# Kernel optimization log

Measured on AMD Instinct MI355X. Metric: run time of the kernel, lower is better.

Reference implementation:

```python
import jax, jax.numpy as jnp
import numpy as np

N2 = 524288   # raw batch (2B)
F = 256       # raw feature dim; concat of halves -> D = 2F
D = 512       # input_dim (gated feature dim)
H_GATE = 64
H_EXP = 128


def _init(key, shape, fan_in):
    return jax.random.normal(key, shape, jnp.float32) / np.sqrt(fan_in)


def setup_inputs() -> dict:
    key = jax.random.key(0)
    ks = jax.random.split(key, 13)
    x = jax.random.normal(ks[0], (N2, F), jnp.float32)
    # gate: Linear(D,64) -> ReLU -> Linear(64,2)
    gw1 = _init(ks[1], (D, H_GATE), D)
    gb1 = jnp.zeros((H_GATE,), jnp.float32)
    gw2 = _init(ks[2], (H_GATE, 2), H_GATE)
    gb2 = jnp.zeros((2,), jnp.float32)
    # expert_a: Linear(D,128) -> ReLU -> Linear(128,2)
    aw1 = _init(ks[3], (D, H_EXP), D)
    ab1 = jnp.zeros((H_EXP,), jnp.float32)
    aw2 = _init(ks[4], (H_EXP, 2), H_EXP)
    ab2 = jnp.zeros((2,), jnp.float32)
    # expert_b: same shapes
    bw1 = _init(ks[5], (D, H_EXP), D)
    bb1 = jnp.zeros((H_EXP,), jnp.float32)
    bw2 = _init(ks[6], (H_EXP, 2), H_EXP)
    bb2 = jnp.zeros((2,), jnp.float32)
    return dict(x=x, gw1=gw1, gb1=gb1, gw2=gw2, gb2=gb2,
                aw1=aw1, ab1=ab1, aw2=aw2, ab2=ab2,
                bw1=bw1, bb1=bb1, bw2=bw2, bb2=bb2)


def reference(x, gw1, gb1, gw2, gb2, aw1, ab1, aw2, ab2, bw1, bb1, bw2, bb2):
    # backbone = identity; concat first and second batch halves along features
    n = x.shape[0]
    xf = jnp.concatenate([x[: n // 2], x[n // 2 :]], axis=1)  # [B, D]
    # hard gate: argmax over 2 logits
    gate_logits = jax.nn.relu(xf @ gw1 + gb1) @ gw2 + gb2  # [B, 2]
    gate_idx = jnp.argmax(gate_logits, axis=1)  # [B]
    # run both tiny experts densely, then mask (same math as masked dispatch)
    out_a = jax.nn.relu(xf @ aw1 + ab1) @ aw2 + ab2  # [B, 2]
    out_b = jax.nn.relu(xf @ bw1 + bb1) @ bw2 + bb2  # [B, 2]
    m_a = (gate_idx == 0)[:, None]
    # rows routed to expert_a fill cols 0:2, rows routed to expert_b fill cols 2:4
    return jnp.concatenate(
        [jnp.where(m_a, out_a, 0.0), jnp.where(m_a, 0.0, out_b)], axis=1
    )  # [B, 4]
```

## Files before the change

kernel.cpp:

```cpp
#include <hip/hip_runtime.h>
#include <hip/hip_bf16.h>

#define HALF_ROWS 262144
#define TAU 0.04f
#define BT_OFF 1024
#define LIST_OFF (BT_OFF + 320 * 512 * 2)

typedef __attribute__((ext_vector_type(8))) short s16x8;
typedef __attribute__((ext_vector_type(4))) unsigned short u16x4;
typedef __attribute__((ext_vector_type(4))) float f32x4;

__device__ __forceinline__ unsigned short f2bf(float f) {
  union { float f; unsigned u; } v; v.f = f;
  unsigned r = v.u + 0x7fffu + ((v.u >> 16) & 1u);
  return (unsigned short)(r >> 16);
}

__global__ void moe_prep(const float* __restrict__ gw1, const float* __restrict__ aw1,
                         const float* __restrict__ bw1, unsigned short* __restrict__ Bf,
                         unsigned* __restrict__ cnt) {
  if (blockIdx.x == 0 && threadIdx.x == 0) *cnt = 0u;
  int idx = blockIdx.x * 512 + threadIdx.x;
  int j = idx & 7, l = (idx >> 3) & 63, ks = (idx >> 9) & 15, cb = idx >> 13;
  int col = cb * 16 + (l & 15);
  int k = ks * 32 + ((l >> 4) << 3) + j;
  float v;
  if (col < 64)       v = gw1[k * 64 + col];
  else if (col < 192) v = aw1[k * 128 + (col - 64)];
  else                v = bw1[k * 128 + (col - 192)];
  Bf[idx] = f2bf(v);
}

__global__ __launch_bounds__(512, 4) void moe_main(
    const float* __restrict__ x, const unsigned short* __restrict__ Bf,
    const float* __restrict__ gb1, const float* __restrict__ gw2, const float* __restrict__ gb2,
    const float* __restrict__ ab1, const float* __restrict__ aw2, const float* __restrict__ ab2,
    const float* __restrict__ bb1, const float* __restrict__ bw2, const float* __restrict__ bb2,
    float* __restrict__ out, unsigned* __restrict__ cnt, unsigned* __restrict__ list, int cap) {
  __shared__ unsigned short A[64 * 512];

  const int tid = threadIdx.x;
  const long br = (long)blockIdx.x * 64;

#pragma unroll 1
  for (int rnd = 0; rnd < 2; ++rnd) {
    f32x4 v[8];
#pragma unroll
    for (int u = 0; u < 8; ++u) {
      int i = tid + (rnd * 8 + u) * 512;
      int row = i >> 7, kq = i & 127;
      long roff = br + row + ((kq >> 6) ? (long)HALF_ROWS : 0L);
      v[u] = *(const f32x4*)(x + roff * 256 + (kq & 63) * 4);
    }
#pragma unroll
    for (int u = 0; u < 8; ++u) {
      int i = tid + (rnd * 8 + u) * 512;
      int row = i >> 7, kq = i & 127;
      u16x4 p;
      p[0] = f2bf(v[u][0]); p[1] = f2bf(v[u][1]);
      p[2] = f2bf(v[u][2]); p[3] = f2bf(v[u][3]);
      int byte = (row * 1024 + kq * 8) ^ ((row & 7) << 4);
      *(u16x4*)((char*)A + byte) = p;
    }
  }
  __syncthreads();

  const int w = tid >> 6, l = tid & 63;
  const int wr = w >> 2, wc = w & 3;
  const int lo = l & 15, hi = l >> 4;

  f32x4 acc[2][5];
#pragma unroll
  for (int i = 0; i < 2; i++)
#pragma unroll
    for (int j = 0; j < 5; j++) acc[i][j] = (f32x4){0.f, 0.f, 0.f, 0.f};

#pragma unroll 2
  for (int ks = 0; ks < 16; ++ks) {
    s16x8 bfr[5], afr[2];
#pragma unroll
    for (int ct = 0; ct < 5; ++ct)
      bfr[ct] = *(const s16x8*)(Bf + (((size_t)((wc * 5 + ct) * 16 + ks)) << 9) + l * 8);
#pragma unroll
    for (int rt = 0; rt < 2; ++rt) {
      int row = wr * 32 + rt * 16 + lo;
      int byte = (row * 1024 + ks * 64 + hi * 16) ^ ((l & 7) << 4);
      afr[rt] = *(const s16x8*)((const char*)A + byte);
    }
#pragma unroll
    for (int rt = 0; rt < 2; ++rt)
#pragma unroll
      for (int ct = 0; ct < 5; ++ct)
        acc[rt][ct] = __builtin_amdgcn_mfma_f32_16x16x32_bf16(
            afr[rt], bfr[ct], acc[rt][ct], 0, 0, 0);
  }
  __syncthreads();

  float* part = (float*)A;
  float b1v[5], w0v[5], w1v[5];
  int head[5];
#pragma unroll
  for (int ct = 0; ct < 5; ++ct) {
    int c0 = wc * 80 + ct * 16;
    int col = c0 + lo;
    int hd = c0 < 64 ? 0 : (c0 < 192 ? 1 : 2);
    head[ct] = hd;
    if (hd == 0)      { b1v[ct] = gb1[col];           w0v[ct] = gw2[col * 2];       w1v[ct] = gw2[col * 2 + 1]; }
    else if (hd == 1) { int c = col - 64;  b1v[ct] = ab1[c]; w0v[ct] = aw2[c * 2]; w1v[ct] = aw2[c * 2 + 1]; }
    else              { int c = col - 192; b1v[ct] = bb1[c]; w0v[ct] = bw2[c * 2]; w1v[ct] = bw2[c * 2 + 1]; }
  }
#pragma unroll
  for (int rt = 0; rt < 2; ++rt) {
    float pg0[4] = {0,0,0,0}, pg1[4] = {0,0,0,0};
    float pa0[4] = {0,0,0,0}, pa1[4] = {0,0,0,0};
    float pq0[4] = {0,0,0,0}, pq1[4] = {0,0,0,0};
#pragma unroll
    for (int ct = 0; ct < 5; ++ct)
#pragma unroll
      for (int j = 0; j < 4; ++j) {
        float h = fmaxf(acc[rt][ct][j] + b1v[ct], 0.f);
        float t0 = h * w0v[ct], t1 = h * w1v[ct];
        if (head[ct] == 0)      { pg0[j] += t0; pg1[j] += t1; }
        else if (head[ct] == 1) { pa0[j] += t0; pa1[j] += t1; }
        else                    { pq0[j] += t0; pq1[j] += t1; }
      }
#pragma unroll
    for (int m = 1; m < 16; m <<= 1)
#pragma unroll
      for (int j = 0; j < 4; ++j) {
        pg0[j] += __shfl_xor(pg0[j], m); pg1[j] += __shfl_xor(pg1[j], m);
        pa0[j] += __shfl_xor(pa0[j], m); pa1[j] += __shfl_xor(pa1[j], m);
        pq0[j] += __shfl_xor(pq0[j], m); pq1[j] += __shfl_xor(pq1[j], m);
      }
    if (lo == 0) {
#pragma unroll
      for (int j = 0; j < 4; ++j) {
        int r = wr * 32 + rt * 16 + hi * 4 + j;
        float* pp = part + (r * 4 + wc) * 6;
        pp[0] = pg0[j]; pp[1] = pg1[j]; pp[2] = pa0[j];
        pp[3] = pa1[j]; pp[4] = pq0[j]; pp[5] = pq1[j];
      }
    }
  }
  __syncthreads();

  if (tid < 64) {
    float g0 = 0, g1 = 0, a0 = 0, a1 = 0, e0 = 0, e1 = 0;
#pragma unroll
    for (int k2 = 0; k2 < 4; k2++) {
      float* pp = part + (tid * 4 + k2) * 6;
      g0 += pp[0]; g1 += pp[1]; a0 += pp[2]; a1 += pp[3]; e0 += pp[4]; e1 += pp[5];
    }
    float gl0 = g0 + gb2[0], gl1 = g1 + gb2[1];
    float fa0 = a0 + ab2[0], fa1 = a1 + ab2[1];
    float fb0 = e0 + bb2[0], fb1 = e1 + bb2[1];
    bool m0 = gl0 >= gl1;
    long grow = br + tid;
    f32x4 o;
    o[0] = m0 ? fa0 : 0.f; o[1] = m0 ? fa1 : 0.f;
    o[2] = m0 ? 0.f : fb0; o[3] = m0 ? 0.f : fb1;
    *(f32x4*)(out + grow * 4) = o;
    float diff = gl0 - gl1;
    if (fabsf(diff) < TAU && cap > 0) {
      unsigned u = atomicAdd(cnt, 1u);
      if (u < (unsigned)cap) {
        unsigned* e = list + (size_t)u * 8;
        e[0] = (unsigned)grow;
        float* ef = (float*)(e + 4);
        ef[0] = fa0; ef[1] = fa1; ef[2] = fb0; ef[3] = fb1;
      }
    }
  }
}

__global__ void moe_fixup(const float* __restrict__ x,
                          const float* __restrict__ gw1, const float* __restrict__ gb1,
                          const float* __restrict__ gw2, const float* __restrict__ gb2,
                          float* __restrict__ out, const unsigned* __restrict__ cnt,
                          const unsigned* __restrict__ list, int cap) {
  unsigned n = *cnt;
  if (n > (unsigned)cap) n = (unsigned)cap;
  const int l = threadIdx.x & 63;
  const int wid = blockIdx.x * (blockDim.x >> 6) + (threadIdx.x >> 6);
  const int nw = gridDim.x * (blockDim.x >> 6);
  for (unsigned e = wid; e < n; e += nw) {
    const unsigned* ent = list + (size_t)e * 8;
    unsigned row = ent[0];
    const float* ef = (const float*)(ent + 4);
    const float* xr0 = x + (long)row * 256;
    const float* xr1 = x + ((long)row + HALF_ROWS) * 256;
    double a0 = 0.0, a1 = 0.0, a2 = 0.0, a3 = 0.0;
#pragma unroll 4
    for (int d = 0; d < 256; d += 4) {
      a0 += (double)xr0[d]     * (double)gw1[d * 64 + l];
      a1 += (double)xr0[d + 1] * (double)gw1[(d + 1) * 64 + l];
      a2 += (double)xr0[d + 2] * (double)gw1[(d + 2) * 64 + l];
      a3 += (double)xr0[d + 3] * (double)gw1[(d + 3) * 64 + l];
    }
#pragma unroll 4
    for (int d = 0; d < 256; d += 4) {
      a0 += (double)xr1[d]     * (double)gw1[(d + 256) * 64 + l];
      a1 += (double)xr1[d + 1] * (double)gw1[(d + 257) * 64 + l];
      a2 += (double)xr1[d + 2] * (double)gw1[(d + 258) * 64 + l];
      a3 += (double)xr1[d + 3] * (double)gw1[(d + 259) * 64 + l];
    }
    double h = a0 + a1 + a2 + a3 + (double)gb1[l];
    h = h > 0.0 ? h : 0.0;
    double t0 = h * (double)gw2[l * 2];
    double t1 = h * (double)gw2[l * 2 + 1];
#pragma unroll
    for (int m = 1; m < 64; m <<= 1) {
      t0 += __shfl_xor(t0, m);
      t1 += __shfl_xor(t1, m);
    }
    if (l == 0) {
      bool m0 = (t0 + (double)gb2[0]) >= (t1 + (double)gb2[1]);
      f32x4 o;
      o[0] = m0 ? ef[0] : 0.f; o[1] = m0 ? ef[1] : 0.f;
      o[2] = m0 ? 0.f : ef[2]; o[3] = m0 ? 0.f : ef[3];
      *(f32x4*)(out + (size_t)row * 4) = o;
    }
  }
}

extern "C" void kernel_launch(void* const* d_in, const int* in_sizes, int n_in,
                              void* d_out, int out_size, void* d_ws, size_t ws_size,
                              hipStream_t stream) {
  const float* x   = (const float*)d_in[0];
  const float* gw1 = (const float*)d_in[1];
  const float* gb1 = (const float*)d_in[2];
  const float* gw2 = (const float*)d_in[3];
  const float* gb2 = (const float*)d_in[4];
  const float* aw1 = (const float*)d_in[5];
  const float* ab1 = (const float*)d_in[6];
  const float* aw2 = (const float*)d_in[7];
  const float* ab2 = (const float*)d_in[8];
  const float* bw1 = (const float*)d_in[9];
  const float* bb1 = (const float*)d_in[10];
  const float* bw2 = (const float*)d_in[11];
  const float* bb2 = (const float*)d_in[12];
  float* out = (float*)d_out;

  unsigned char* ws = (unsigned char*)d_ws;
  unsigned* cnt = (unsigned*)ws;
  unsigned short* Bf = (unsigned short*)(ws + BT_OFF);
  unsigned* list = (unsigned*)(ws + LIST_OFF);
  long cap_l = ((long)ws_size - (long)LIST_OFF) / 32;
  int cap = cap_l < 0 ? 0 : (cap_l > 262144 ? 262144 : (int)cap_l);

  moe_prep<<<320, 512, 0, stream>>>(gw1, aw1, bw1, Bf, cnt);
  moe_main<<<4096, 512, 0, stream>>>(x, Bf, gb1, gw2, gb2, ab1, aw2, ab2,
                                     bb1, bw2, bb2, out, cnt, list, cap);
  moe_fixup<<<1024, 256, 0, stream>>>(x, gw1, gb1, gw2, gb2, out, cnt, list, cap);
}
```

Before: 311.6 us.

## Make moe_main persistent over eight panels with register-prefetch of next panel

Each block now handles eight consecutive 64-row panels instead of one, and the grid shrinks to 512 blocks. The next panel's x tile is loaded into registers while the current panel's MFMA and epilogue run, then converted and written to LDS afterwards. The aim is to hide global load latency behind compute and to amortize per-block setup such as the bias and weight loads. In exchange it holds 16 extra f32x4 registers per thread, lowers launch bounds to 2 blocks per CU, and uses fewer blocks, which may leave CUs under-filled.

```diff
diff --git a/kernel.cpp b/kernel.cpp
--- a/kernel.cpp
+++ b/kernel.cpp
@@ -31,72 +31,21 @@
   Bf[idx] = f2bf(v);
 }
 
-__global__ __launch_bounds__(512, 4) void moe_main(
+__global__ __launch_bounds__(512, 2) void moe_main(
     const float* __restrict__ x, const unsigned short* __restrict__ Bf,
     const float* __restrict__ gb1, const float* __restrict__ gw2, const float* __restrict__ gb2,
     const float* __restrict__ ab1, const float* __restrict__ aw2, const float* __restrict__ ab2,
     const float* __restrict__ bb1, const float* __restrict__ bw2, const float* __restrict__ bb2,
     float* __restrict__ out, unsigned* __restrict__ cnt, unsigned* __restrict__ list, int cap) {
   __shared__ unsigned short A[64 * 512];
+  __shared__ float part[64 * 4 * 6];
 
   const int tid = threadIdx.x;
-  const long br = (long)blockIdx.x * 64;
-
-#pragma unroll 1
-  for (int rnd = 0; rnd < 2; ++rnd) {
-    f32x4 v[8];
-#pragma unroll
-    for (int u = 0; u < 8; ++u) {
-      int i = tid + (rnd * 8 + u) * 512;
-      int row = i >> 7, kq = i & 127;
-      long roff = br + row + ((kq >> 6) ? (long)HALF_ROWS : 0L);
-      v[u] = *(const f32x4*)(x + roff * 256 + (kq & 63) * 4);
-    }
-#pragma unroll
-    for (int u = 0; u < 8; ++u) {
-      int i = tid + (rnd * 8 + u) * 512;
-      int row = i >> 7, kq = i & 127;
-      u16x4 p;
-      p[0] = f2bf(v[u][0]); p[1] = f2bf(v[u][1]);
-      p[2] = f2bf(v[u][2]); p[3] = f2bf(v[u][3]);
-      int byte = (row * 1024 + kq * 8) ^ ((row & 7) << 4);
-      *(u16x4*)((char*)A + byte) = p;
-    }
-  }
-  __syncthreads();
-
   const int w = tid >> 6, l = tid & 63;
   const int wr = w >> 2, wc = w & 3;
   const int lo = l & 15, hi = l >> 4;
-
-  f32x4 acc[2][5];
-#pragma unroll
-  for (int i = 0; i < 2; i++)
-#pragma unroll
-    for (int j = 0; j < 5; j++) acc[i][j] = (f32x4){0.f, 0.f, 0.f, 0.f};
-
-#pragma unroll 2
-  for (int ks = 0; ks < 16; ++ks) {
-    s16x8 bfr[5], afr[2];
-#pragma unroll
-    for (int ct = 0; ct < 5; ++ct)
-      bfr[ct] = *(const s16x8*)(Bf + (((size_t)((wc * 5 + ct) * 16 + ks)) << 9) + l * 8);
-#pragma unroll
-    for (int rt = 0; rt < 2; ++rt) {
-      int row = wr * 32 + rt * 16 + lo;
-      int byte = (row * 1024 + ks * 64 + hi * 16) ^ ((l & 7) << 4);
-      afr[rt] = *(const s16x8*)((const char*)A + byte);
-    }
-#pragma unroll
-    for (int rt = 0; rt < 2; ++rt)
-#pragma unroll
-      for (int ct = 0; ct < 5; ++ct)
-        acc[rt][ct] = __builtin_amdgcn_mfma_f32_16x16x32_bf16(
-            afr[rt], bfr[ct], acc[rt][ct], 0, 0, 0);
-  }
-  __syncthreads();
-
-  float* part = (float*)A;
+  const int p0 = blockIdx.x * 8;
+
   float b1v[5], w0v[5], w1v[5];
   int head[5];
 #pragma unroll
@@ -109,67 +58,132 @@
     else if (hd == 1) { int c = col - 64;  b1v[ct] = ab1[c]; w0v[ct] = aw2[c * 2]; w1v[ct] = aw2[c * 2 + 1]; }
     else              { int c = col - 192; b1v[ct] = bb1[c]; w0v[ct] = bw2[c * 2]; w1v[ct] = bw2[c * 2 + 1]; }
   }
-#pragma unroll
-  for (int rt = 0; rt < 2; ++rt) {
-    float pg0[4] = {0,0,0,0}, pg1[4] = {0,0,0,0};
-    float pa0[4] = {0,0,0,0}, pa1[4] = {0,0,0,0};
-    float pq0[4] = {0,0,0,0}, pq1[4] = {0,0,0,0};
-#pragma unroll
-    for (int ct = 0; ct < 5; ++ct)
-#pragma unroll
-      for (int j = 0; j < 4; ++j) {
-        float h = fmaxf(acc[rt][ct][j] + b1v[ct], 0.f);
-        float t0 = h * w0v[ct], t1 = h * w1v[ct];
-        if (head[ct] == 0)      { pg0[j] += t0; pg1[j] += t1; }
-        else if (head[ct] == 1) { pa0[j] += t0; pa1[j] += t1; }
-        else                    { pq0[j] += t0; pq1[j] += t1; }
-      }
-#pragma unroll
-    for (int m = 1; m < 16; m <<= 1)
-#pragma unroll
-      for (int j = 0; j < 4; ++j) {
-        pg0[j] += __shfl_xor(pg0[j], m); pg1[j] += __shfl_xor(pg1[j], m);
-        pa0[j] += __shfl_xor(pa0[j], m); pa1[j] += __shfl_xor(pa1[j], m);
-        pq0[j] += __shfl_xor(pq0[j], m); pq1[j] += __shfl_xor(pq1[j], m);
-      }
-    if (lo == 0) {
-#pragma unroll
-      for (int j = 0; j < 4; ++j) {
-        int r = wr * 32 + rt * 16 + hi * 4 + j;
-        float* pp = part + (r * 4 + wc) * 6;
-        pp[0] = pg0[j]; pp[1] = pg1[j]; pp[2] = pa0[j];
-        pp[3] = pa1[j]; pp[4] = pq0[j]; pp[5] = pq1[j];
-      }
-    }
-  }
+
+  f32x4 st[16];
+  auto issueP = [&](int panel) {
+    long br = (long)panel * 64;
+#pragma unroll
+    for (int u = 0; u < 16; ++u) {
+      int i = tid + u * 512;
+      int row = i >> 7, kq = i & 127;
+      long roff = br + row + ((kq >> 6) ? (long)HALF_ROWS : 0L);
+      st[u] = *(const f32x4*)(x + roff * 256 + (kq & 63) * 4);
+    }
+  };
+  auto commitP = [&]() {
+#pragma unroll
+    for (int u = 0; u < 16; ++u) {
+      int i = tid + u * 512;
+      int row = i >> 7, kq = i & 127;
+      u16x4 p4;
+      p4[0] = f2bf(st[u][0]); p4[1] = f2bf(st[u][1]);
+      p4[2] = f2bf(st[u][2]); p4[3] = f2bf(st[u][3]);
+      int byte = (row * 1024 + kq * 8) ^ ((row & 7) << 4);
+      *(u16x4*)((char*)A + byte) = p4;
+    }
+  };
+
+  issueP(p0);
+  commitP();
   __syncthreads();
 
-  if (tid < 64) {
-    float g0 = 0, g1 = 0, a0 = 0, a1 = 0, e0 = 0, e1 = 0;
-#pragma unroll
-    for (int k2 = 0; k2 < 4; k2++) {
-      float* pp = part + (tid * 4 + k2) * 6;
-      g0 += pp[0]; g1 += pp[1]; a0 += pp[2]; a1 += pp[3]; e0 += pp[4]; e1 += pp[5];
-    }
-    float gl0 = g0 + gb2[0], gl1 = g1 + gb2[1];
-    float fa0 = a0 + ab2[0], fa1 = a1 + ab2[1];
-    float fb0 = e0 + bb2[0], fb1 = e1 + bb2[1];
-    bool m0 = gl0 >= gl1;
-    long grow = br + tid;
-    f32x4 o;
-    o[0] = m0 ? fa0 : 0.f; o[1] = m0 ? fa1 : 0.f;
-    o[2] = m0 ? 0.f : fb0; o[3] = m0 ? 0.f : fb1;
-    *(f32x4*)(out + grow * 4) = o;
-    float diff = gl0 - gl1;
-    if (fabsf(diff) < TAU && cap > 0) {
-      unsigned u = atomicAdd(cnt, 1u);
-      if (u < (unsigned)cap) {
-        unsigned* e = list + (size_t)u * 8;
-        e[0] = (unsigned)grow;
-        float* ef = (float*)(e + 4);
-        ef[0] = fa0; ef[1] = fa1; ef[2] = fb0; ef[3] = fb1;
-      }
-    }
+#pragma unroll 1
+  for (int pp = 0; pp < 8; ++pp) {
+    const int panel = p0 + pp;
+    const long br = (long)panel * 64;
+    const bool hasNext = pp < 7;
+    if (hasNext) issueP(panel + 1);
+
+    f32x4 acc[2][5];
+#pragma unroll
+    for (int i = 0; i < 2; i++)
+#pragma unroll
+      for (int j = 0; j < 5; j++) acc[i][j] = (f32x4){0.f, 0.f, 0.f, 0.f};
+
+#pragma unroll 4
+    for (int ks = 0; ks < 16; ++ks) {
+      s16x8 bfr[5], afr[2];
+#pragma unroll
+      for (int ct = 0; ct < 5; ++ct)
+        bfr[ct] = *(const s16x8*)(Bf + (((size_t)((wc * 5 + ct) * 16 + ks)) << 9) + l * 8);
+#pragma unroll
+      for (int rt = 0; rt < 2; ++rt) {
+        int row = wr * 32 + rt * 16 + lo;
+        int byte = (row * 1024 + ks * 64 + hi * 16) ^ ((l & 7) << 4);
+        afr[rt] = *(const s16x8*)((const char*)A + byte);
+      }
+#pragma unroll
+      for (int rt = 0; rt < 2; ++rt)
+#pragma unroll
+        for (int ct = 0; ct < 5; ++ct)
+          acc[rt][ct] = __builtin_amdgcn_mfma_f32_16x16x32_bf16(
+              afr[rt], bfr[ct], acc[rt][ct], 0, 0, 0);
+    }
+
+#pragma unroll
+    for (int rt = 0; rt < 2; ++rt) {
+      float pg0[4] = {0,0,0,0}, pg1[4] = {0,0,0,0};
+      float pa0[4] = {0,0,0,0}, pa1[4] = {0,0,0,0};
+      float pq0[4] = {0,0,0,0}, pq1[4] = {0,0,0,0};
+#pragma unroll
+      for (int ct = 0; ct < 5; ++ct)
+#pragma unroll
+        for (int j = 0; j < 4; ++j) {
+          float h = fmaxf(acc[rt][ct][j] + b1v[ct], 0.f);
+          float t0 = h * w0v[ct], t1 = h * w1v[ct];
+          if (head[ct] == 0)      { pg0[j] += t0; pg1[j] += t1; }
+          else if (head[ct] == 1) { pa0[j] += t0; pa1[j] += t1; }
+          else                    { pq0[j] += t0; pq1[j] += t1; }
+        }
+#pragma unroll
+      for (int m = 1; m < 16; m <<= 1)
+#pragma unroll
+        for (int j = 0; j < 4; ++j) {
+          pg0[j] += __shfl_xor(pg0[j], m); pg1[j] += __shfl_xor(pg1[j], m);
+          pa0[j] += __shfl_xor(pa0[j], m); pa1[j] += __shfl_xor(pa1[j], m);
+          pq0[j] += __shfl_xor(pq0[j], m); pq1[j] += __shfl_xor(pq1[j], m);
+        }
+      if (lo == 0) {
+#pragma unroll
+        for (int j = 0; j < 4; ++j) {
+          int r = wr * 32 + rt * 16 + hi * 4 + j;
+          float* pp2 = part + (r * 4 + wc) * 6;
+          pp2[0] = pg0[j]; pp2[1] = pg1[j]; pp2[2] = pa0[j];
+          pp2[3] = pa1[j]; pp2[4] = pq0[j]; pp2[5] = pq1[j];
+        }
+      }
+    }
+    __syncthreads();
+
+    if (tid < 64) {
+      float g0 = 0, g1 = 0, a0 = 0, a1 = 0, e0 = 0, e1 = 0;
+#pragma unroll
+      for (int k2 = 0; k2 < 4; k2++) {
+        float* pp2 = part + (tid * 4 + k2) * 6;
+        g0 += pp2[0]; g1 += pp2[1]; a0 += pp2[2]; a1 += pp2[3]; e0 += pp2[4]; e1 += pp2[5];
+      }
+      float gl0 = g0 + gb2[0], gl1 = g1 + gb2[1];
+      float fa0 = a0 + ab2[0], fa1 = a1 + ab2[1];
+      float fb0 = e0 + bb2[0], fb1 = e1 + bb2[1];
+      bool m0 = gl0 >= gl1;
+      long grow = br + tid;
+      f32x4 o;
+      o[0] = m0 ? fa0 : 0.f; o[1] = m0 ? fa1 : 0.f;
+      o[2] = m0 ? 0.f : fb0; o[3] = m0 ? 0.f : fb1;
+      *(f32x4*)(out + grow * 4) = o;
+      float diff = gl0 - gl1;
+      if (fabsf(diff) < TAU && cap > 0) {
+        unsigned u = atomicAdd(cnt, 1u);
+        if (u < (unsigned)cap) {
+          unsigned* e = list + (size_t)u * 8;
+          e[0] = (unsigned)grow;
+          float* ef = (float*)(e + 4);
+          ef[0] = fa0; ef[1] = fa1; ef[2] = fb0; ef[3] = fb1;
+        }
+      }
+    }
+    if (hasNext) commitP();
+    __syncthreads();
   }
 }
 
@@ -249,7 +263,7 @@
   int cap = cap_l < 0 ? 0 : (cap_l > 262144 ? 262144 : (int)cap_l);
 
   moe_prep<<<320, 512, 0, stream>>>(gw1, aw1, bw1, Bf, cnt);
-  moe_main<<<4096, 512, 0, stream>>>(x, Bf, gb1, gw2, gb2, ab1, aw2, ab2,
-                                     bb1, bw2, bb2, out, cnt, list, cap);
+  moe_main<<<512, 512, 0, stream>>>(x, Bf, gb1, gw2, gb2, ab1, aw2, ab2,
+                                    bb1, bw2, bb2, out, cnt, list, cap);
   moe_fixup<<<1024, 256, 0, stream>>>(x, gw1, gb1, gw2, gb2, out, cnt, list, cap);
 }
```

Result: slower. 394.8 us (+26.7%).

## Pipeline K-chunks with register-prefetched A and async global-to-LDS B loads

Applied to the files above, without the earlier changes.

The kernel no longer stages the whole 64x512 A tile in shared memory before computing. It now loops over 8 K-chunks. B fragments are copied straight from global into LDS with global_load_lds, and the next A chunk is prefetched into registers while the current chunk runs MFMA. Shared memory drops from 64KB to 48KB, which could allow more resident blocks and overlaps load latency with compute. In exchange it adds two barriers per chunk and relies on hand-written waitcnt values being correct.

```diff
diff --git a/kernel.cpp b/kernel.cpp
--- a/kernel.cpp
+++ b/kernel.cpp
@@ -7,7 +7,7 @@
 #define LIST_OFF (BT_OFF + 320 * 512 * 2)
 
 typedef __attribute__((ext_vector_type(8))) short s16x8;
-typedef __attribute__((ext_vector_type(4))) unsigned short u16x4;
+typedef __attribute__((ext_vector_type(8))) unsigned short u16x8;
 typedef __attribute__((ext_vector_type(4))) float f32x4;
 
 __device__ __forceinline__ unsigned short f2bf(float f) {
@@ -15,6 +15,10 @@
   unsigned r = v.u + 0x7fffu + ((v.u >> 16) & 1u);
   return (unsigned short)(r >> 16);
 }
+
+#define GLOAD_LDS16(g, p) \
+  __builtin_amdgcn_global_load_lds((const __attribute__((address_space(1))) void*)(g), \
+                                   (__attribute__((address_space(3))) void*)(p), 16, 0, 0)
 
 __global__ void moe_prep(const float* __restrict__ gw1, const float* __restrict__ aw1,
                          const float* __restrict__ bw1, unsigned short* __restrict__ Bf,
@@ -37,37 +41,36 @@
     const float* __restrict__ ab1, const float* __restrict__ aw2, const float* __restrict__ ab2,
     const float* __restrict__ bb1, const float* __restrict__ bw2, const float* __restrict__ bb2,
     float* __restrict__ out, unsigned* __restrict__ cnt, unsigned* __restrict__ list, int cap) {
-  __shared__ unsigned short A[64 * 512];
+  __shared__ char L[49152];
+  char* ALb = L;
+  char* BLb = L + 8192;
+  float* part = (float*)L;
 
   const int tid = threadIdx.x;
-  const long br = (long)blockIdx.x * 64;
-
-#pragma unroll 1
-  for (int rnd = 0; rnd < 2; ++rnd) {
-    f32x4 v[8];
-#pragma unroll
-    for (int u = 0; u < 8; ++u) {
-      int i = tid + (rnd * 8 + u) * 512;
-      int row = i >> 7, kq = i & 127;
-      long roff = br + row + ((kq >> 6) ? (long)HALF_ROWS : 0L);
-      v[u] = *(const f32x4*)(x + roff * 256 + (kq & 63) * 4);
-    }
-#pragma unroll
-    for (int u = 0; u < 8; ++u) {
-      int i = tid + (rnd * 8 + u) * 512;
-      int row = i >> 7, kq = i & 127;
-      u16x4 p;
-      p[0] = f2bf(v[u][0]); p[1] = f2bf(v[u][1]);
-      p[2] = f2bf(v[u][2]); p[3] = f2bf(v[u][3]);
-      int byte = (row * 1024 + kq * 8) ^ ((row & 7) << 4);
-      *(u16x4*)((char*)A + byte) = p;
-    }
-  }
-  __syncthreads();
-
+  const int bid = blockIdx.x;
   const int w = tid >> 6, l = tid & 63;
   const int wr = w >> 2, wc = w & 3;
   const int lo = l & 15, hi = l >> 4;
+  const long br = (long)bid * 64;
+
+  const int arow = ((tid >> 7) << 4) + (tid & 15);
+  const int akl  = ((tid >> 6) & 1) * 32 + ((tid >> 4) & 3) * 8;
+
+  f32x4 sa0, sa1;
+  auto issueA = [&](int kc) {
+    const float* p = x + ((long)(kc >= 4 ? HALF_ROWS : 0) + br + arow) * 256
+                       + (kc & 3) * 64 + akl;
+    sa0 = *(const f32x4*)p;
+    sa1 = *(const f32x4*)(p + 4);
+  };
+  auto commitA = [&]() {
+    u16x8 u;
+    const float* s0 = (const float*)&sa0;
+    const float* s1 = (const float*)&sa1;
+#pragma unroll
+    for (int i = 0; i < 4; ++i) { u[i] = f2bf(s0[i]); u[4 + i] = f2bf(s1[i]); }
+    *(u16x8*)(ALb + (size_t)tid * 16) = u;
+  };
 
   f32x4 acc[2][5];
 #pragma unroll
@@ -75,33 +78,51 @@
 #pragma unroll
     for (int j = 0; j < 5; j++) acc[i][j] = (f32x4){0.f, 0.f, 0.f, 0.f};
 
-#pragma unroll 2
-  for (int ks = 0; ks < 16; ++ks) {
-    s16x8 bfr[5], afr[2];
-#pragma unroll
-    for (int ct = 0; ct < 5; ++ct)
-      bfr[ct] = *(const s16x8*)(Bf + (((size_t)((wc * 5 + ct) * 16 + ks)) << 9) + l * 8);
-#pragma unroll
-    for (int rt = 0; rt < 2; ++rt) {
-      int row = wr * 32 + rt * 16 + lo;
-      int byte = (row * 1024 + ks * 64 + hi * 16) ^ ((l & 7) << 4);
-      afr[rt] = *(const s16x8*)((const char*)A + byte);
-    }
-#pragma unroll
-    for (int rt = 0; rt < 2; ++rt)
+  issueA(0);
+
+#pragma unroll 1
+  for (int kc = 0; kc < 8; ++kc) {
+#pragma unroll
+    for (int s5 = 0; s5 < 5; ++s5) {
+      int s = w * 5 + s5;
+      const unsigned short* g = Bf + ((size_t)(((s >> 1) * 16 + kc * 2 + (s & 1)) * 64 + l)) * 8;
+      GLOAD_LDS16(g, BLb + (size_t)s * 1024);
+    }
+    asm volatile("" ::: "memory");
+    commitA();
+    if (kc < 7) {
+      issueA(kc + 1);
+      asm volatile("s_waitcnt vmcnt(2) lgkmcnt(0)" ::: "memory");
+    } else {
+      asm volatile("s_waitcnt vmcnt(0) lgkmcnt(0)" ::: "memory");
+    }
+    __builtin_amdgcn_s_barrier();
+
+#pragma unroll
+    for (int ks = 0; ks < 2; ++ks) {
+      s16x8 afr[2], bfr[5];
+#pragma unroll
+      for (int rt = 0; rt < 2; ++rt)
+        afr[rt] = *(const s16x8*)(ALb + (size_t)((((wr * 2 + rt) * 2 + ks) * 64 + l)) * 16);
 #pragma unroll
       for (int ct = 0; ct < 5; ++ct)
-        acc[rt][ct] = __builtin_amdgcn_mfma_f32_16x16x32_bf16(
-            afr[rt], bfr[ct], acc[rt][ct], 0, 0, 0);
-  }
-  __syncthreads();
-
-  float* part = (float*)A;
+        bfr[ct] = *(const s16x8*)(BLb + (size_t)((((wc * 5 + ct) * 2 + ks) * 64 + l)) * 16);
+#pragma unroll
+      for (int rt = 0; rt < 2; ++rt)
+#pragma unroll
+        for (int ct = 0; ct < 5; ++ct)
+          acc[rt][ct] = __builtin_amdgcn_mfma_f32_16x16x32_bf16(
+              afr[rt], bfr[ct], acc[rt][ct], 0, 0, 0);
+    }
+    asm volatile("" ::: "memory");
+    __builtin_amdgcn_s_barrier();
+  }
+
   float b1v[5], w0v[5], w1v[5];
   int head[5];
 #pragma unroll
   for (int ct = 0; ct < 5; ++ct) {
-    int c0 = wc * 80 + ct * 16;
+    int c0 = (wc * 5 + ct) * 16;
     int col = c0 + lo;
     int hd = c0 < 64 ? 0 : (c0 < 192 ? 1 : 2);
     head[ct] = hd;
```

After: 307.2 us. About the same (-1.4%).
